# Performance work log

Measured on AMD Instinct MI355X. Metric: run time of the kernel, lower is better.

## Reference

```python
import jax, jax.numpy as jnp
import numpy as np

DIM = 1024
NUM_HEADS = 16
HEAD_DIM = DIM // NUM_HEADS
CHUNK = 128
SCALE = HEAD_DIM ** -0.5
RMS_EPS_BIT = 1.1920929e-07  # torch.finfo(float32).eps (nn.RMSNorm default)
RMS_EPS_OUT = 1e-6


def activation_quant(x):
    scale = 127.0 / jnp.clip(jnp.max(jnp.abs(x), axis=-1, keepdims=True), 1e-5)
    return jnp.clip(jnp.round(x * scale), -128, 127) / scale


def weight_quant(w):
    scale = 1.0 / jnp.clip(jnp.mean(jnp.abs(w)), 1e-5)
    return jnp.clip(jnp.round(w * scale), -1, 1) / scale


def bitlinear(x, w, b, norm_w):
    xn = x * jax.lax.rsqrt(jnp.mean(x * x, axis=-1, keepdims=True) + RMS_EPS_BIT) * norm_w
    xq = xn + jax.lax.stop_gradient(activation_quant(xn) - xn)
    wq = w + jax.lax.stop_gradient(weight_quant(w) - w)
    return xq @ wq.T + b


def rms_norm(x, w):
    return x * jax.lax.rsqrt(jnp.mean(x * x, axis=-1, keepdims=True) + RMS_EPS_OUT) * w


def apply_rope(x, cos, sin):
    # x: [B,N,H,D]; cos/sin: [N, D//2]
    B, N, H, D = x.shape
    cos_e = jnp.repeat(cos[:N], 2, axis=-1)[None, :, None, :]  # [1,N,1,D]
    sin_e = jnp.repeat(sin[:N], 2, axis=-1)[None, :, None, :]
    xh = x.reshape(B, N, H, D // 2, 2)
    x_rot = jnp.stack([-xh[..., 1], xh[..., 0]], axis=-1).reshape(B, N, H, D)
    return x * cos_e + x_rot * sin_e


def setup_inputs() -> dict:
    key = jax.random.key(0)
    ks = jax.random.split(key, 8)
    B, N = 2, 8192
    return {
        "x": jax.random.normal(ks[0], (B, N, DIM), jnp.float32),
        "cos": jax.random.uniform(ks[1], (N, HEAD_DIM // 2), jnp.float32),
        "sin": jax.random.uniform(ks[2], (N, HEAD_DIM // 2), jnp.float32),
        "qkv_w": jax.random.normal(ks[3], (3 * DIM, DIM), jnp.float32) * 0.02,
        "qkv_b": jnp.zeros((3 * DIM,), jnp.float32),
        "qkv_nw": jnp.ones((DIM,), jnp.float32),
        "proj_w": jax.random.normal(ks[4], (DIM, DIM), jnp.float32) * 0.02,
        "proj_b": jnp.zeros((DIM,), jnp.float32),
        "proj_nw": jnp.ones((DIM,), jnp.float32),
        "norm_w": jnp.ones((DIM,), jnp.float32),
    }


def lightning_attention(x, cos, sin, qkv_w, qkv_b, qkv_nw, proj_w, proj_b, proj_nw, norm_w):
    B, N, C = x.shape
    qkv = bitlinear(x, qkv_w, qkv_b, qkv_nw).reshape(B, N, 3, NUM_HEADS, HEAD_DIM)
    q, k, v = qkv[:, :, 0], qkv[:, :, 1], qkv[:, :, 2]
    q = apply_rope(q, cos, sin)
    k = apply_rope(k, cos, sin)
    # N chosen as a multiple of CHUNK (pad_len == 0)
    T = N // CHUNK
    # [T, B, chunk, H, Dh]
    qc = jnp.moveaxis(q.reshape(B, T, CHUNK, NUM_HEADS, HEAD_DIM), 1, 0)
    kc = jnp.moveaxis(k.reshape(B, T, CHUNK, NUM_HEADS, HEAD_DIM), 1, 0)
    vc = jnp.moveaxis(v.reshape(B, T, CHUNK, NUM_HEADS, HEAD_DIM), 1, 0)
    causal = jnp.tril(jnp.ones((CHUNK, CHUNK), bool))
    neg_inf = jnp.finfo(x.dtype).min

    def step(kv_state, chunk):
        q_t, k_t, v_t = chunk  # each [B, chunk, H, Dh]
        scores = jnp.einsum('bqhd,bkhd->bhqk', q_t, k_t) * SCALE
        scores = jnp.where(causal, scores, neg_inf)
        attn = jax.nn.softmax(scores, axis=-1)
        o_intra = jnp.einsum('bhqk,bkhd->bqhd', attn, v_t)
        o_inter = jnp.einsum('bqhd,bhde->bqhe', q_t, kv_state)
        kv_new = kv_state + jnp.einsum('bkhd,bkhe->bhde', k_t, v_t)
        return kv_new, o_intra + o_inter

    kv0 = jnp.zeros((B, NUM_HEADS, HEAD_DIM, HEAD_DIM), x.dtype)
    _, out = jax.lax.scan(step, kv0, (qc, kc, vc))  # out: [T,B,chunk,H,Dh]
    out = jnp.moveaxis(out, 0, 1).reshape(B, N, C)
    return bitlinear(rms_norm(out, norm_w), proj_w, proj_b, proj_nw)


def reference(x, cos, sin, qkv_w, qkv_b, qkv_nw, proj_w, proj_b, proj_nw, norm_w):
    return lightning_attention(x, cos, sin, qkv_w, qkv_b, qkv_nw, proj_w, proj_b, proj_nw, norm_w)
```

## Files before the change

kernel.cpp:

```cpp
#include <hip/hip_runtime.h>


typedef unsigned short USH;
typedef __attribute__((ext_vector_type(8))) short short8;
typedef __attribute__((ext_vector_type(4))) float f32x4;
typedef __attribute__((ext_vector_type(4))) USH us4;

__device__ __forceinline__ float b2f(USH u) { return __uint_as_float(((unsigned)u) << 16); }
__device__ __forceinline__ USH f2b(float f) {
    unsigned u = __float_as_uint(f);
    u += 0x7fffu + ((u >> 16) & 1u);
    return (USH)(u >> 16);
}
__device__ __forceinline__ f32x4 mfma16(short8 a, short8 b, f32x4 c) {
    return __builtin_amdgcn_mfma_f32_16x16x32_bf16(a, b, c, 0, 0, 0);
}
__device__ __forceinline__ void gload_lds16(const void* g, void* l) {
    __builtin_amdgcn_global_load_lds(
        (const __attribute__((address_space(1))) unsigned*)g,
        (__attribute__((address_space(3))) unsigned*)l, 16, 0, 0);
}

__device__ __forceinline__ float blk_sum(float v, float* red) {
#pragma unroll
    for (int o = 32; o; o >>= 1) v += __shfl_xor(v, o);
    __syncthreads();
    if ((threadIdx.x & 63) == 0) red[threadIdx.x >> 6] = v;
    __syncthreads();
    return red[0] + red[1] + red[2] + red[3];
}
__device__ __forceinline__ float blk_max(float v, float* red) {
#pragma unroll
    for (int o = 32; o; o >>= 1) v = fmaxf(v, __shfl_xor(v, o));
    __syncthreads();
    if ((threadIdx.x & 63) == 0) red[threadIdx.x >> 6] = v;
    __syncthreads();
    return fmaxf(fmaxf(red[0], red[1]), fmaxf(red[2], red[3]));
}

__global__ __launch_bounds__(256) void k_wabs(const float* __restrict__ qw,
                                              const float* __restrict__ pw,
                                              float* __restrict__ partials) {
    __shared__ float red[4];
    int which = blockIdx.y;
    const float4* p = (const float4*)(which ? pw : qw);
    int n4 = which ? (1024 * 1024 / 4) : (3072 * 1024 / 4);
    float s = 0.f;
    for (int i = blockIdx.x * 256 + threadIdx.x; i < n4; i += 256 * 256) {
        float4 v = p[i];
        s += fabsf(v.x) + fabsf(v.y) + fabsf(v.z) + fabsf(v.w);
    }
#pragma unroll
    for (int o = 32; o; o >>= 1) s += __shfl_xor(s, o);
    if ((threadIdx.x & 63) == 0) red[threadIdx.x >> 6] = s;
    __syncthreads();
    if (threadIdx.x == 0)
        partials[which * 256 + blockIdx.x] = red[0] + red[1] + red[2] + red[3];
}

__global__ __launch_bounds__(256) void k_wsum(const float* __restrict__ partials,
                                              float* __restrict__ sums) {
    __shared__ double red[4];
    int which = blockIdx.x;
    double v = (double)partials[which * 256 + threadIdx.x];
#pragma unroll
    for (int o = 32; o; o >>= 1) v += __shfl_xor(v, o);
    if ((threadIdx.x & 63) == 0) red[threadIdx.x >> 6] = v;
    __syncthreads();
    if (threadIdx.x == 0)
        sums[which] = (float)(red[0] + red[1] + red[2] + red[3]);
}

__global__ __launch_bounds__(256) void k_wquant(const float* __restrict__ qw,
                                                const float* __restrict__ pw,
                                                const float* __restrict__ sums,
                                                USH* __restrict__ wqk, USH* __restrict__ wqp) {
    int id = blockIdx.x * 256 + threadIdx.x;
    float4 v; USH* dst; float sc;
    if (id < 786432) {
        v = ((const float4*)qw)[id];
        sc = 1.f / fmaxf(sums[0] * (1.f / 3145728.f), 1e-5f);
        dst = wqk + (size_t)id * 4;
    } else {
        int j = id - 786432;
        v = ((const float4*)pw)[j];
        sc = 1.f / fmaxf(sums[1] * (1.f / 1048576.f), 1e-5f);
        dst = wqp + (size_t)j * 4;
    }
    us4 o;
    o.x = f2b(fminf(fmaxf(rintf(v.x * sc), -1.f), 1.f));
    o.y = f2b(fminf(fmaxf(rintf(v.y * sc), -1.f), 1.f));
    o.z = f2b(fminf(fmaxf(rintf(v.z * sc), -1.f), 1.f));
    o.w = f2b(fminf(fmaxf(rintf(v.w * sc), -1.f), 1.f));
    *(us4*)dst = o;
}

__global__ __launch_bounds__(256) void k_actq(const float* __restrict__ x,
                                              const float* __restrict__ nw,
                                              USH* __restrict__ xq, float* __restrict__ inva) {
    __shared__ float red[4];
    int row = blockIdx.x, tid = threadIdx.x;
    float4 v = ((const float4*)(x + (size_t)row * 1024))[tid];
    float4 w = ((const float4*)nw)[tid];
    float ss = v.x * v.x + v.y * v.y + v.z * v.z + v.w * v.w;
    ss = blk_sum(ss, red);
    float r1 = rsqrtf(ss * (1.f / 1024.f) + 1.1920929e-07f);
    float x0 = v.x * r1 * w.x, x1 = v.y * r1 * w.y, x2 = v.z * r1 * w.z, x3 = v.w * r1 * w.w;
    float am = fmaxf(fmaxf(fabsf(x0), fabsf(x1)), fmaxf(fabsf(x2), fabsf(x3)));
    am = blk_max(am, red);
    float amc = fmaxf(am, 1e-5f);
    float sc = 127.f / amc;
    us4 o;
    o.x = f2b(fminf(fmaxf(rintf(x0 * sc), -128.f), 127.f));
    o.y = f2b(fminf(fmaxf(rintf(x1 * sc), -128.f), 127.f));
    o.z = f2b(fminf(fmaxf(rintf(x2 * sc), -128.f), 127.f));
    o.w = f2b(fminf(fmaxf(rintf(x3 * sc), -128.f), 127.f));
    *(us4*)(xq + (size_t)row * 1024 + tid * 4) = o;
    if (tid == 0) inva[row] = amc * (1.f / 127.f);
}

__global__ __launch_bounds__(256) void k_norm2q(const USH* __restrict__ oat,
                                                const float* __restrict__ nw,
                                                const float* __restrict__ pnw,
                                                USH* __restrict__ xq, float* __restrict__ inva) {
    __shared__ float red[4];
    int row = blockIdx.x, tid = threadIdx.x;
    us4 ov = *(const us4*)(oat + (size_t)row * 1024 + tid * 4);
    float o0 = b2f(ov.x), o1 = b2f(ov.y), o2 = b2f(ov.z), o3 = b2f(ov.w);
    float4 w = ((const float4*)nw)[tid];
    float4 pw = ((const float4*)pnw)[tid];
    float ss1 = blk_sum(o0 * o0 + o1 * o1 + o2 * o2 + o3 * o3, red);
    float r1 = rsqrtf(ss1 * (1.f / 1024.f) + 1e-6f);
    float y0 = o0 * r1 * w.x, y1 = o1 * r1 * w.y, y2 = o2 * r1 * w.z, y3 = o3 * r1 * w.w;
    float ss2 = blk_sum(y0 * y0 + y1 * y1 + y2 * y2 + y3 * y3, red);
    float r2 = rsqrtf(ss2 * (1.f / 1024.f) + 1.1920929e-07f);
    float z0 = y0 * r2 * pw.x, z1 = y1 * r2 * pw.y, z2 = y2 * r2 * pw.z, z3 = y3 * r2 * pw.w;
    float am = fmaxf(fmaxf(fabsf(z0), fabsf(z1)), fmaxf(fabsf(z2), fabsf(z3)));
    am = blk_max(am, red);
    float amc = fmaxf(am, 1e-5f);
    float sc = 127.f / amc;
    us4 q;
    q.x = f2b(fminf(fmaxf(rintf(z0 * sc), -128.f), 127.f));
    q.y = f2b(fminf(fmaxf(rintf(z1 * sc), -128.f), 127.f));
    q.z = f2b(fminf(fmaxf(rintf(z2 * sc), -128.f), 127.f));
    q.w = f2b(fminf(fmaxf(rintf(z3 * sc), -128.f), 127.f));
    *(us4*)(xq + (size_t)row * 1024 + tid * 4) = q;
    if (tid == 0) inva[row] = amc * (1.f / 127.f);
}

template <bool OUT_BF16>
__global__ __launch_bounds__(256) void k_gemm(const USH* __restrict__ A, const USH* __restrict__ W,
                                              const float* __restrict__ inva,
                                              const float* __restrict__ wsum, float wcnt,
                                              const float* __restrict__ bias,
                                              void* __restrict__ out, int Nn, int K) {
    __shared__ USH As[128 * 64];
    __shared__ USH Bs[128 * 64];
    int tid = threadIdx.x;
    int wv = tid >> 6, lane = tid & 63, quad = lane >> 4, lid = lane & 15;
    int bn = blockIdx.x, bm = blockIdx.y;
    f32x4 acc[2][8];
#pragma unroll
    for (int mt = 0; mt < 2; mt++)
#pragma unroll
        for (int nt = 0; nt < 8; nt++)
#pragma unroll
            for (int r = 0; r < 4; r++) acc[mt][nt][r] = 0.f;

    const USH* Ag = A + (size_t)(bm * 128 + wv * 32 + (lane >> 3)) * K + (lane & 7) * 8;
    const USH* Wg = W + (size_t)(bn * 128 + wv * 32 + (lane >> 3)) * K + (lane & 7) * 8;

    for (int kk = 0; kk < K; kk += 64) {
        if (kk) __syncthreads();
#pragma unroll
        for (int i = 0; i < 4; i++) {
            gload_lds16(Ag + (size_t)(i * 8) * K + kk, &As[(wv * 32 + i * 8) * 64]);
            gload_lds16(Wg + (size_t)(i * 8) * K + kk, &Bs[(wv * 32 + i * 8) * 64]);
        }
        __syncthreads();
#pragma unroll
        for (int ksx = 0; ksx < 2; ksx++) {
            int co = ksx * 32 + quad * 8;
            short8 af[2], bf[8];
            af[0] = *(const short8*)&As[(wv * 32 + lid) * 64 + co];
            af[1] = *(const short8*)&As[(wv * 32 + 16 + lid) * 64 + co];
#pragma unroll
            for (int nt = 0; nt < 8; nt++) bf[nt] = *(const short8*)&Bs[(nt * 16 + lid) * 64 + co];
#pragma unroll
            for (int mt = 0; mt < 2; mt++)
#pragma unroll
                for (int nt = 0; nt < 8; nt++) acc[mt][nt] = mfma16(af[mt], bf[nt], acc[mt][nt]);
        }
    }
    float wm = fmaxf(wsum[0] * (1.f / wcnt), 1e-5f);
#pragma unroll
    for (int mt = 0; mt < 2; mt++)
#pragma unroll
        for (int r = 0; r < 4; r++) {
            int rowg = bm * 128 + wv * 32 + mt * 16 + quad * 4 + r;
            float ia = inva[rowg] * wm;
#pragma unroll
            for (int nt = 0; nt < 8; nt++) {
                int colg = bn * 128 + nt * 16 + lid;
                float v = acc[mt][nt][r] * ia + bias[colg];
                if (OUT_BF16) ((USH*)out)[(size_t)rowg * Nn + colg] = f2b(v);
                else ((float*)out)[(size_t)rowg * Nn + colg] = v;
            }
        }
}

__global__ __launch_bounds__(256) void k_rope(USH* __restrict__ qkv,
                                              const float* __restrict__ cs,
                                              const float* __restrict__ sn) {
    int id = blockIdx.x * 256 + threadIdx.x;
    int rowm = id >> 10, p = id & 1023;
    int part = p >> 9, pi = p & 511;
    int h = pi >> 5, i = pi & 31;
    int n = rowm & 8191;
    size_t a = (size_t)rowm * 3072 + part * 1024 + h * 64 + 2 * i;
    float c = cs[n * 32 + i], s = sn[n * 32 + i];
    unsigned* pp = (unsigned*)(qkv + a);
    unsigned u = *pp;
    float x0 = b2f((USH)(u & 0xffff)), x1 = b2f((USH)(u >> 16));
    float y0 = x0 * c - x1 * s;
    float y1 = x1 * c + x0 * s;
    *pp = (unsigned)f2b(y0) | ((unsigned)f2b(y1) << 16);
}

__global__ __launch_bounds__(256) void k_attn_intra(const USH* __restrict__ qkv,
                                                    USH* __restrict__ oat) {
    __shared__ char smem[36864 + 17408];
    USH* qs = (USH*)smem;
    USH* kqs = qs + 128 * 72;
    USH* Ps = (USH*)smem;
    USH* vt = (USH*)(smem + 36864);
    int tid = threadIdx.x, wv = tid >> 6, lane = tid & 63, quad = lane >> 4, lid = lane & 15;
    int t = blockIdx.x, bh = blockIdx.y, b = bh >> 4, h = bh & 15;
    size_t base = ((size_t)(b * 8192 + t * 128)) * 3072 + h * 64;
    int r0 = tid >> 3, c0 = (tid & 7) * 8;
#pragma unroll
    for (int i = 0; i < 4; i++) {
        int r = i * 32 + r0;
        short8 qv = *(const short8*)(qkv + base + (size_t)r * 3072 + c0);
        short8 kv = *(const short8*)(qkv + base + (size_t)r * 3072 + 1024 + c0);
        short8 vv = *(const short8*)(qkv + base + (size_t)r * 3072 + 2048 + c0);
        *(short8*)&qs[r * 72 + c0] = qv;
        *(short8*)&kqs[r * 72 + c0] = kv;
        USH tmp[8]; *(short8*)tmp = vv;
#pragma unroll
        for (int j = 0; j < 8; j++) vt[(c0 + j) * 136 + r] = tmp[j];
    }
    __syncthreads();

    f32x4 accs[2][8];
#pragma unroll
    for (int mt = 0; mt < 2; mt++)
#pragma unroll
        for (int nt = 0; nt < 8; nt++)
#pragma unroll
            for (int r = 0; r < 4; r++) accs[mt][nt][r] = 0.f;
    int R = wv * 32;
#pragma unroll
    for (int ksx = 0; ksx < 2; ksx++) {
        int co = ksx * 32 + quad * 8;
        short8 af0 = *(const short8*)&qs[(R + lid) * 72 + co];
        short8 af1 = *(const short8*)&qs[(R + 16 + lid) * 72 + co];
        short8 bf[8];
#pragma unroll
        for (int nt = 0; nt < 8; nt++) bf[nt] = *(const short8*)&kqs[(nt * 16 + lid) * 72 + co];
#pragma unroll
        for (int nt = 0; nt < 8; nt++) {
            accs[0][nt] = mfma16(af0, bf[nt], accs[0][nt]);
            accs[1][nt] = mfma16(af1, bf[nt], accs[1][nt]);
        }
    }
#pragma unroll
    for (int mt = 0; mt < 2; mt++)
#pragma unroll
        for (int r = 0; r < 4; r++) {
            int row = R + mt * 16 + quad * 4 + r;
            float sv[8];
            float mx = -3.0e38f;
#pragma unroll
            for (int nt = 0; nt < 8; nt++) {
                int col = nt * 16 + lid;
                float v = accs[mt][nt][r] * 0.125f;
                sv[nt] = (col <= row) ? v : -3.0e38f;
                mx = fmaxf(mx, sv[nt]);
            }
#pragma unroll
            for (int o = 8; o; o >>= 1) mx = fmaxf(mx, __shfl_xor(mx, o));
            float sm = 0.f;
#pragma unroll
            for (int nt = 0; nt < 8; nt++) {
                float e = (sv[nt] > -1.0e38f) ? __expf(sv[nt] - mx) : 0.f;
                sv[nt] = e; sm += e;
            }
#pragma unroll
            for (int o = 8; o; o >>= 1) sm += __shfl_xor(sm, o);
            float inv = 1.f / sm;
#pragma unroll
            for (int nt = 0; nt < 8; nt++) accs[mt][nt][r] = sv[nt] * inv;
        }
    __syncthreads();
#pragma unroll
    for (int mt = 0; mt < 2; mt++)
#pragma unroll
        for (int nt = 0; nt < 8; nt++)
#pragma unroll
            for (int r = 0; r < 4; r++)
                Ps[(R + mt * 16 + quad * 4 + r) * 136 + nt * 16 + lid] = f2b(accs[mt][nt][r]);
    __syncthreads();

    f32x4 acco[8];
#pragma unroll
    for (int nt = 0; nt < 8; nt++)
#pragma unroll
        for (int r = 0; r < 4; r++) acco[nt][r] = 0.f;
#pragma unroll
    for (int kq = 0; kq < 4; kq++) {
        int co = kq * 32 + quad * 8;
        short8 av = *(const short8*)&vt[(wv * 16 + lid) * 136 + co];
#pragma unroll
        for (int nt = 0; nt < 8; nt++) {
            short8 bp = *(const short8*)&Ps[(nt * 16 + lid) * 136 + co];
            acco[nt] = mfma16(av, bp, acco[nt]);
        }
    }
    size_t obase = (size_t)(b * 8192 + t * 128) * 1024 + h * 64;
#pragma unroll
    for (int nt = 0; nt < 8; nt++)
#pragma unroll
        for (int r = 0; r < 4; r++) {
            int d = wv * 16 + quad * 4 + r;
            int q = nt * 16 + lid;
            oat[obase + (size_t)q * 1024 + d] = f2b(acco[nt][r]);
        }
}

__global__ __launch_bounds__(256) void k_kvchunk(const USH* __restrict__ qkv,
                                                 float* __restrict__ kvc) {
    __shared__ char smem[2 * 17408];
    USH* kt = (USH*)smem;
    USH* vt = (USH*)(smem + 17408);
    int tid = threadIdx.x, wv = tid >> 6, lane = tid & 63, quad = lane >> 4, lid = lane & 15;
    int t = blockIdx.x, bh = blockIdx.y, b = bh >> 4, h = bh & 15;
    size_t base = ((size_t)(b * 8192 + t * 128)) * 3072 + h * 64;
    int r0 = tid >> 3, c0 = (tid & 7) * 8;
#pragma unroll
    for (int i = 0; i < 4; i++) {
        int r = i * 32 + r0;
        short8 kv = *(const short8*)(qkv + base + (size_t)r * 3072 + 1024 + c0);
        short8 vv = *(const short8*)(qkv + base + (size_t)r * 3072 + 2048 + c0);
        USH tk[8]; *(short8*)tk = kv;
        USH tv[8]; *(short8*)tv = vv;
#pragma unroll
        for (int j = 0; j < 8; j++) {
            kt[(c0 + j) * 136 + r] = tk[j];
            vt[(c0 + j) * 136 + r] = tv[j];
        }
    }
    __syncthreads();
    f32x4 acc[4];
#pragma unroll
    for (int nt = 0; nt < 4; nt++)
#pragma unroll
        for (int r = 0; r < 4; r++) acc[nt][r] = 0.f;
#pragma unroll
    for (int kq = 0; kq < 4; kq++) {
        int co = kq * 32 + quad * 8;
        short8 ak = *(const short8*)&kt[(wv * 16 + lid) * 136 + co];
#pragma unroll
        for (int nt = 0; nt < 4; nt++) {
            short8 bv = *(const short8*)&vt[(nt * 16 + lid) * 136 + co];
            acc[nt] = mfma16(ak, bv, acc[nt]);
        }
    }
    float* out = kvc + ((size_t)bh * 64 + t) * 4096;
#pragma unroll
    for (int nt = 0; nt < 4; nt++)
#pragma unroll
        for (int r = 0; r < 4; r++) {
            int d = wv * 16 + quad * 4 + r, e = nt * 16 + lid;
            out[d * 64 + e] = acc[nt][r];
        }
}

__global__ __launch_bounds__(256) void k_prefix(float* __restrict__ kvc) {
    int gid = blockIdx.x * 256 + threadIdx.x;
    int bh = gid >> 12, idx = gid & 4095;
    float* p = kvc + (size_t)bh * 64 * 4096 + idx;
    float a = 0.f;
    for (int t = 0; t < 64; t++) {
        float c = p[(size_t)t * 4096];
        p[(size_t)t * 4096] = a;
        a += c;
    }
}

__global__ __launch_bounds__(256) void k_ointer(const USH* __restrict__ qkv,
                                                const float* __restrict__ kvc,
                                                USH* __restrict__ oat) {
    __shared__ char smem[18432 + 9216];
    USH* qs = (USH*)smem;
    USH* kvt = (USH*)(smem + 18432);
    int tid = threadIdx.x, wv = tid >> 6, lane = tid & 63, quad = lane >> 4, lid = lane & 15;
    int t = blockIdx.x, bh = blockIdx.y, b = bh >> 4, h = bh & 15;
    size_t base = ((size_t)(b * 8192 + t * 128)) * 3072 + h * 64;
    int r0 = tid >> 3, c0 = (tid & 7) * 8;
#pragma unroll
    for (int i = 0; i < 4; i++) {
        int r = i * 32 + r0;
        short8 qv = *(const short8*)(qkv + base + (size_t)r * 3072 + c0);
        *(short8*)&qs[r * 72 + c0] = qv;
    }
    const float* kv = kvc + ((size_t)bh * 64 + t) * 4096;
#pragma unroll
    for (int j = 0; j < 16; j++) {
        int idx = j * 256 + tid;
        int d = idx >> 6, e = idx & 63;
        kvt[e * 72 + d] = f2b(kv[idx]);
    }
    __syncthreads();
    f32x4 acc[2][4];
#pragma unroll
    for (int mt = 0; mt < 2; mt++)
#pragma unroll
        for (int nt = 0; nt < 4; nt++)
#pragma unroll
            for (int r = 0; r < 4; r++) acc[mt][nt][r] = 0.f;
    int R = wv * 32;
#pragma unroll
    for (int kd = 0; kd < 2; kd++) {
        int co = kd * 32 + quad * 8;
        short8 a0 = *(const short8*)&qs[(R + lid) * 72 + co];
        short8 a1 = *(const short8*)&qs[(R + 16 + lid) * 72 + co];
#pragma unroll
        for (int nt = 0; nt < 4; nt++) {
            short8 bv = *(const short8*)&kvt[(nt * 16 + lid) * 72 + co];
            acc[0][nt] = mfma16(a0, bv, acc[0][nt]);
            acc[1][nt] = mfma16(a1, bv, acc[1][nt]);
        }
    }
#pragma unroll
    for (int mt = 0; mt < 2; mt++)
#pragma unroll
        for (int nt = 0; nt < 4; nt++)
#pragma unroll
            for (int r = 0; r < 4; r++) {
                int row = t * 128 + R + mt * 16 + quad * 4 + r;
                size_t idx = ((size_t)b * 8192 + row) * 1024 + h * 64 + nt * 16 + lid;
                float prev = b2f(oat[idx]);
                oat[idx] = f2b(prev + acc[mt][nt][r]);
            }
}

extern "C" void kernel_launch(void* const* d_in, const int* in_sizes, int n_in,
                              void* d_out, int out_size, void* d_ws, size_t ws_size,
                              hipStream_t stream) {
    const float* x      = (const float*)d_in[0];
    const float* cosp   = (const float*)d_in[1];
    const float* sinp   = (const float*)d_in[2];
    const float* qkv_w  = (const float*)d_in[3];
    const float* qkv_b  = (const float*)d_in[4];
    const float* qkv_nw = (const float*)d_in[5];
    const float* proj_w = (const float*)d_in[6];
    const float* proj_b = (const float*)d_in[7];
    const float* proj_nw= (const float*)d_in[8];
    const float* norm_w = (const float*)d_in[9];
    float* out = (float*)d_out;

    char* w = (char*)d_ws;
    float* sums    = (float*)(w + 0);
    float* partials= (float*)(w + 64);
    USH*   wq_qkv  = (USH*)(w + 4096);
    USH*   wq_proj = (USH*)(w + 4096 + 6291456);
    float* inva    = (float*)(w + 8392704);
    char*  R1      = w + 8458240;
    char*  R2      = w + 8458240 + 33554432;
    USH*   qkv     = (USH*)(w + 8458240 + 2ull * 33554432);
    USH*   xq      = (USH*)R1;
    USH*   oat     = (USH*)R1;
    float* kvc     = (float*)R2;
    USH*   xq2     = (USH*)R2;

    k_wabs<<<dim3(256, 2), 256, 0, stream>>>(qkv_w, proj_w, partials);
    k_wsum<<<2, 256, 0, stream>>>(partials, sums);
    k_wquant<<<4096, 256, 0, stream>>>(qkv_w, proj_w, sums, wq_qkv, wq_proj);
    k_actq<<<16384, 256, 0, stream>>>(x, qkv_nw, xq, inva);
    k_gemm<true><<<dim3(24, 128), 256, 0, stream>>>(xq, wq_qkv, inva, &sums[0], 3145728.f,
                                                    qkv_b, (void*)qkv, 3072, 1024);
    k_rope<<<65536, 256, 0, stream>>>(qkv, cosp, sinp);
    k_attn_intra<<<dim3(64, 32), 256, 0, stream>>>(qkv, oat);
    k_kvchunk<<<dim3(64, 32), 256, 0, stream>>>(qkv, kvc);
    k_prefix<<<512, 256, 0, stream>>>(kvc);
    k_ointer<<<dim3(64, 32), 256, 0, stream>>>(qkv, kvc, oat);
    k_norm2q<<<16384, 256, 0, stream>>>(oat, norm_w, proj_nw, xq2, inva);
    k_gemm<false><<<dim3(8, 128), 256, 0, stream>>>(xq2, wq_proj, inva, &sums[1], 1048576.f,
                                                    proj_b, (void*)out, 1024, 1024);
    (void)in_sizes; (void)n_in; (void)out_size; (void)ws_size;
}
```

Baseline: 503.0 us.

## Rewrite GEMM with 256x256 tiles, triple-buffered LDS pipeline and swizzled layout

Reworks the bitlinear GEMM kernel to use 512-thread blocks with 256x256 output tiles, a three-stage LDS ring buffer with asynchronous global-to-LDS prefetch two steps ahead, XOR-swizzled LDS layout, block-id swizzling for L2 locality, and s_setprio around MFMA bursts. It aims to hide global load latency behind MFMA work, raise arithmetic intensity per tile, and cut LDS bank conflicts. The risk is higher register pressure from 32 accumulators per thread, and fewer blocks (768 and 256), which could underfill the 256 CUs for the projection GEMM.

```diff
diff --git a/kernel.cpp b/kernel.cpp
--- a/kernel.cpp
+++ b/kernel.cpp
@@ -149,59 +149,112 @@
 }
 
 template <bool OUT_BF16>
-__global__ __launch_bounds__(256) void k_gemm(const USH* __restrict__ A, const USH* __restrict__ W,
-                                              const float* __restrict__ inva,
-                                              const float* __restrict__ wsum, float wcnt,
-                                              const float* __restrict__ bias,
-                                              void* __restrict__ out, int Nn, int K) {
-    __shared__ USH As[128 * 64];
-    __shared__ USH Bs[128 * 64];
-    int tid = threadIdx.x;
-    int wv = tid >> 6, lane = tid & 63, quad = lane >> 4, lid = lane & 15;
-    int bn = blockIdx.x, bm = blockIdx.y;
-    f32x4 acc[2][8];
-#pragma unroll
-    for (int mt = 0; mt < 2; mt++)
-#pragma unroll
-        for (int nt = 0; nt < 8; nt++)
+__global__ __launch_bounds__(512, 2) void k_gemm(const USH* __restrict__ A, const USH* __restrict__ W,
+                                                 const float* __restrict__ inva,
+                                                 const float* __restrict__ wsum, float wcnt,
+                                                 const float* __restrict__ bias,
+                                                 void* __restrict__ out, int Nn, int K) {
+    __shared__ __align__(16) USH lds[3 * 16384];
+    const int tid = threadIdx.x;
+    const int wv = tid >> 6, lane = tid & 63, quad = lane >> 4, lid = lane & 15;
+    const int wr = wv >> 2, wc = wv & 3;
+
+    const int nbn = gridDim.x;
+    const int nwg = nbn * gridDim.y;
+    const int bid = blockIdx.y * nbn + blockIdx.x;
+    const int swb = (bid & 7) * (nwg >> 3) + (bid >> 3);
+    const int bn = swb % nbn, bm = swb / nbn;
+
+    const int T = K >> 5;
+
+    const USH* ag[2]; const USH* wg[2];
+#pragma unroll
+    for (int j = 0; j < 2; j++) {
+        int r = (j * 8 + wv) * 16 + (lane >> 2);
+        int sw = (r & 3) ^ ((r >> 2) & 1);
+        int c16 = (lane & 3) ^ sw;
+        ag[j] = A + (size_t)(bm * 256 + r) * K + c16 * 8;
+        wg[j] = W + (size_t)(bn * 256 + r) * K + c16 * 8;
+    }
+    const int sq = quad ^ ((lid & 3) ^ ((lid >> 2) & 1));
+    const int arow = (wr * 128 + lid) * 32 + sq * 8;
+    const int brow = (wc * 64 + lid) * 32 + sq * 8;
+
+    f32x4 acc[8][4];
+#pragma unroll
+    for (int mt = 0; mt < 8; mt++)
+#pragma unroll
+        for (int nt = 0; nt < 4; nt++)
 #pragma unroll
             for (int r = 0; r < 4; r++) acc[mt][nt][r] = 0.f;
 
-    const USH* Ag = A + (size_t)(bm * 128 + wv * 32 + (lane >> 3)) * K + (lane & 7) * 8;
-    const USH* Wg = W + (size_t)(bn * 128 + wv * 32 + (lane >> 3)) * K + (lane & 7) * 8;
-
-    for (int kk = 0; kk < K; kk += 64) {
-        if (kk) __syncthreads();
-#pragma unroll
-        for (int i = 0; i < 4; i++) {
-            gload_lds16(Ag + (size_t)(i * 8) * K + kk, &As[(wv * 32 + i * 8) * 64]);
-            gload_lds16(Wg + (size_t)(i * 8) * K + kk, &Bs[(wv * 32 + i * 8) * 64]);
-        }
-        __syncthreads();
-#pragma unroll
-        for (int ksx = 0; ksx < 2; ksx++) {
-            int co = ksx * 32 + quad * 8;
-            short8 af[2], bf[8];
-            af[0] = *(const short8*)&As[(wv * 32 + lid) * 64 + co];
-            af[1] = *(const short8*)&As[(wv * 32 + 16 + lid) * 64 + co];
-#pragma unroll
-            for (int nt = 0; nt < 8; nt++) bf[nt] = *(const short8*)&Bs[(nt * 16 + lid) * 64 + co];
-#pragma unroll
-            for (int mt = 0; mt < 2; mt++)
-#pragma unroll
-                for (int nt = 0; nt < 8; nt++) acc[mt][nt] = mfma16(af[mt], bf[nt], acc[mt][nt]);
-        }
-    }
+#pragma unroll
+    for (int t = 0; t < 2; t++) {
+        USH* dst = &lds[t * 16384];
+#pragma unroll
+        for (int j = 0; j < 2; j++) {
+            gload_lds16(ag[j] + t * 32, &dst[(j * 8 + wv) * 512]);
+            gload_lds16(wg[j] + t * 32, &dst[8192 + (j * 8 + wv) * 512]);
+        }
+    }
+
+    for (int t = 0; t < T; ++t) {
+        const USH* As = &lds[(t % 3) * 16384];
+        const USH* Bs = As + 8192;
+        USH* Pd = &lds[((t + 2) % 3) * 16384];
+        short8 af[8], bf[4];
+        if (t + 1 < T) asm volatile("s_waitcnt vmcnt(4) lgkmcnt(0)" ::: "memory");
+        else           asm volatile("s_waitcnt vmcnt(0) lgkmcnt(0)" ::: "memory");
+        __builtin_amdgcn_s_barrier();
+        __builtin_amdgcn_sched_barrier(0);
+        asm volatile("" ::: "memory");
+        if (t + 2 < T) {
+#pragma unroll
+            for (int j = 0; j < 2; j++)
+                gload_lds16(ag[j] + (t + 2) * 32, &Pd[(j * 8 + wv) * 512]);
+        }
+#pragma unroll
+        for (int mt = 0; mt < 4; mt++)
+            af[mt] = *(const short8*)&As[arow + mt * 512];
+#pragma unroll
+        for (int nt = 0; nt < 4; nt++)
+            bf[nt] = *(const short8*)&Bs[brow + nt * 512];
+        __builtin_amdgcn_s_setprio(1);
+#pragma unroll
+        for (int mt = 0; mt < 4; mt++)
+#pragma unroll
+            for (int nt = 0; nt < 4; nt++) acc[mt][nt] = mfma16(af[mt], bf[nt], acc[mt][nt]);
+        __builtin_amdgcn_s_setprio(0);
+        asm volatile("s_waitcnt lgkmcnt(0)" ::: "memory");
+        __builtin_amdgcn_s_barrier();
+        __builtin_amdgcn_sched_barrier(0);
+        asm volatile("" ::: "memory");
+        if (t + 2 < T) {
+#pragma unroll
+            for (int j = 0; j < 2; j++)
+                gload_lds16(wg[j] + (t + 2) * 32, &Pd[8192 + (j * 8 + wv) * 512]);
+        }
+#pragma unroll
+        for (int mt = 4; mt < 8; mt++)
+            af[mt] = *(const short8*)&As[arow + mt * 512];
+        __builtin_amdgcn_s_setprio(1);
+#pragma unroll
+        for (int mt = 4; mt < 8; mt++)
+#pragma unroll
+            for (int nt = 0; nt < 4; nt++) acc[mt][nt] = mfma16(af[mt], bf[nt], acc[mt][nt]);
+        __builtin_amdgcn_s_setprio(0);
+    }
+
     float wm = fmaxf(wsum[0] * (1.f / wcnt), 1e-5f);
 #pragma unroll
-    for (int mt = 0; mt < 2; mt++)
+    for (int mt = 0; mt < 8; mt++)
 #pragma unroll
         for (int r = 0; r < 4; r++) {
-            int rowg = bm * 128 + wv * 32 + mt * 16 + quad * 4 + r;
+            int rowg = bm * 256 + wr * 128 + mt * 16 + quad * 4 + r;
             float ia = inva[rowg] * wm;
 #pragma unroll
-            for (int nt = 0; nt < 8; nt++) {
-                int colg = bn * 128 + nt * 16 + lid;
+            for (int nt = 0; nt < 4; nt++) {
+                int colg = bn * 256 + wc * 64 + nt * 16 + lid;
                 float v = acc[mt][nt][r] * ia + bias[colg];
                 if (OUT_BF16) ((USH*)out)[(size_t)rowg * Nn + colg] = f2b(v);
                 else ((float*)out)[(size_t)rowg * Nn + colg] = v;
@@ -488,15 +541,15 @@
     k_wsum<<<2, 256, 0, stream>>>(partials, sums);
     k_wquant<<<4096, 256, 0, stream>>>(qkv_w, proj_w, sums, wq_qkv, wq_proj);
     k_actq<<<16384, 256, 0, stream>>>(x, qkv_nw, xq, inva);
-    k_gemm<true><<<dim3(24, 128), 256, 0, stream>>>(xq, wq_qkv, inva, &sums[0], 3145728.f,
-                                                    qkv_b, (void*)qkv, 3072, 1024);
+    k_gemm<true><<<dim3(12, 64), 512, 0, stream>>>(xq, wq_qkv, inva, &sums[0], 3145728.f,
+                                                   qkv_b, (void*)qkv, 3072, 1024);
     k_rope<<<65536, 256, 0, stream>>>(qkv, cosp, sinp);
     k_attn_intra<<<dim3(64, 32), 256, 0, stream>>>(qkv, oat);
     k_kvchunk<<<dim3(64, 32), 256, 0, stream>>>(qkv, kvc);
     k_prefix<<<512, 256, 0, stream>>>(kvc);
     k_ointer<<<dim3(64, 32), 256, 0, stream>>>(qkv, kvc, oat);
     k_norm2q<<<16384, 256, 0, stream>>>(oat, norm_w, proj_nw, xq2, inva);
-    k_gemm<false><<<dim3(8, 128), 256, 0, stream>>>(xq2, wq_proj, inva, &sums[1], 1048576.f,
-                                                    proj_b, (void*)out, 1024, 1024);
+    k_gemm<false><<<dim3(4, 64), 512, 0, stream>>>(xq2, wq_proj, inva, &sums[1], 1048576.f,
+                                                   proj_b, (void*)out, 1024, 1024);
     (void)in_sizes; (void)n_in; (void)out_size; (void)ws_size;
 }
```

New measurement: 445.6 us. -11.4%, faster.
